# Kernel tuning notes

Hardware: AMD Instinct MI355X
Metric: run time of the kernel (lower is better)

The kernel has to match this reference:

```python
import jax, jax.numpy as jnp
import numpy as np

B, C, N = 16, 256, 8192          # batch, channels, points
CN, CL = 128, 64                 # curve_num, curve_length
MID = C // 2
BN_EPS = 1e-5


def setup_inputs() -> dict:
    key = jax.random.key(0)
    ks = jax.random.split(key, 10)
    def w(k, shape, fan_in):  # kaiming-ish init for 1x1 conv weights
        return jax.random.normal(k, shape, jnp.float32) * np.float32(1.0 / np.sqrt(fan_in))
    return {
        "x": jax.random.normal(ks[0], (B, C, N), jnp.float32),
        "curves": jax.random.normal(ks[1], (B, C, CN, CL), jnp.float32),
        "w_att": w(ks[2], (1, C), C),        # line_conv_att (Conv2d C->1, 1x1)
        "wa": w(ks[3], (MID, C), C),         # conva
        "wb": w(ks[4], (MID, C), C),         # convb
        "wc": w(ks[5], (MID, C), C),         # convc
        "wn": w(ks[6], (MID, MID), MID),     # convn
        "wl": w(ks[7], (MID, MID), MID),     # convl
        "wd": w(ks[8], (C, 2 * MID), 2 * MID),  # convd conv
        "bn_gamma": jnp.ones((C,), jnp.float32),
        "bn_beta": jnp.zeros((C,), jnp.float32),
        "bn_mean": jnp.zeros((C,), jnp.float32),
        "bn_var": jnp.ones((C,), jnp.float32),
    }


def reference(x, curves, w_att, wa, wb, wc, wn, wl, wd,
              bn_gamma, bn_beta, bn_mean, bn_var):
    # curves: [B, C, n, l]; attention logits over curves via 1x1 conv C->1
    att = jnp.einsum('oc,bcnl->bnl', w_att, curves)              # [B, n, l]
    # inter: softmax over curve_length (l); intra: softmax over curve_num (n)
    curver_inter = jnp.einsum('bcnl,bnl->bcn', curves, jax.nn.softmax(att, axis=-1))  # [B,C,n]
    curves_intra = jnp.einsum('bcnl,bnl->bcl', curves, jax.nn.softmax(att, axis=-2))  # [B,C,l]

    a = jnp.einsum('mc,bcn->bmn', wa, curver_inter)              # [B, mid, n]
    b = jnp.einsum('mc,bcl->bml', wb, curves_intra)              # [B, mid, l]
    x_logits = jnp.einsum('mc,bcp->bpm', wc, x)                  # [B, N, mid]

    x_inter = jax.nn.softmax(jnp.einsum('bpm,bmn->bpn', x_logits, a), axis=-1)  # [B,N,n]
    x_intra = jax.nn.softmax(jnp.einsum('bpm,bml->bpl', x_logits, b), axis=-1)  # [B,N,l]

    an = jnp.einsum('om,bmn->bno', wn, a)                        # [B, n, mid]
    bl = jnp.einsum('om,bml->blo', wl, b)                        # [B, l, mid]

    xi = jnp.einsum('bpn,bnm->bpm', x_inter, an)                 # [B, N, mid]
    xt = jnp.einsum('bpl,blm->bpm', x_intra, bl)                 # [B, N, mid]

    feat = jnp.concatenate((xi, xt), axis=-1)                    # [B, N, 2*mid]
    y = jnp.einsum('cd,bpd->bcp', wd, feat)                      # [B, C, N]
    # BatchNorm1d (inference mode: running stats)
    scale = (bn_gamma / jnp.sqrt(bn_var + BN_EPS))[None, :, None]
    y = (y - bn_mean[None, :, None]) * scale + bn_beta[None, :, None]
    return jax.nn.leaky_relu(x + y, 0.2)
```

## Files before the change

### kernel.cpp

```cpp
#include <hip/hip_runtime.h>
#include <hip/hip_bf16.h>
#include <cstdint>

#define B_   16
#define C_   256
#define N_   8192
#define CN_  128
#define CL_  64
#define MID_ 128

typedef unsigned short u16;
typedef __attribute__((ext_vector_type(8))) short bf8;
typedef __attribute__((ext_vector_type(4))) float f4;

#define MFMA(a, bb, c) __builtin_amdgcn_mfma_f32_16x16x32_bf16(a, bb, c, 0, 0, 0)

#define BAR() do {                                        \
    __builtin_amdgcn_sched_barrier(0);                    \
    asm volatile("s_waitcnt lgkmcnt(0)" ::: "memory");    \
    __builtin_amdgcn_s_barrier();                         \
    __builtin_amdgcn_sched_barrier(0);                    \
  } while (0)

__device__ inline u16 f2b(float v) {
  uint32_t b = __builtin_bit_cast(uint32_t, v);
  uint32_t r = (b + 0x7FFFu + ((b >> 16) & 1u)) >> 16;
  return (u16)r;
}
__device__ inline float b2f(u16 u) {
  uint32_t b = ((uint32_t)u) << 16;
  return __builtin_bit_cast(float, b);
}
__device__ inline void st4(u16* p, u16 a, u16 b, u16 c, u16 d) {
  unsigned long long v = (unsigned long long)a | ((unsigned long long)b << 16) |
                         ((unsigned long long)c << 32) | ((unsigned long long)d << 48);
  *(unsigned long long*)p = v;
}

__global__ __launch_bounds__(256) void k_wfold(const float* __restrict__ wd,
                                               const float* __restrict__ wn,
                                               const float* __restrict__ wl,
                                               float* __restrict__ wdnT,
                                               float* __restrict__ wdlT) {
  const int idx = blockIdx.x * 256 + threadIdx.x;
  const int plane = idx >> 15;
  const int r = idx & 32767;
  const int c = r & 255, m = r >> 8;
  const float* wsrc = plane ? wl : wn;
  const float* wdrow = wd + c * 256 + plane * 128;
  float a0 = 0.f, a1 = 0.f, a2 = 0.f, a3 = 0.f;
  for (int o = 0; o < 128; o += 4) {
    a0 = fmaf(wdrow[o + 0], wsrc[(o + 0) * 128 + m], a0);
    a1 = fmaf(wdrow[o + 1], wsrc[(o + 1) * 128 + m], a1);
    a2 = fmaf(wdrow[o + 2], wsrc[(o + 2) * 128 + m], a2);
    a3 = fmaf(wdrow[o + 3], wsrc[(o + 3) * 128 + m], a3);
  }
  (plane ? wdlT : wdnT)[m * 256 + c] = (a0 + a1) + (a2 + a3);
}

__global__ __launch_bounds__(256) void k_wfold2(
    const float* __restrict__ wa, const float* __restrict__ wb,
    const float* __restrict__ wc,
    const float* __restrict__ wdnT, const float* __restrict__ wdlT,
    float* __restrict__ Wac, float* __restrict__ Wna,
    float* __restrict__ Wbc, float* __restrict__ Wlb) {
  const int idx = blockIdx.x * 256 + threadIdx.x;
  const int quad = idx >> 16;
  const int r = idx & 65535;
  const int cc = r & 255, c = r >> 8;
  const float* L = (quad & 2) ? wb : wa;
  const float* R = (quad & 1) ? ((quad & 2) ? wdlT : wdnT) : wc;
  float a0 = 0.f, a1 = 0.f, a2 = 0.f, a3 = 0.f;
  for (int m = 0; m < 128; m += 4) {
    a0 = fmaf(L[(m + 0) * 256 + c], R[(m + 0) * 256 + cc], a0);
    a1 = fmaf(L[(m + 1) * 256 + c], R[(m + 1) * 256 + cc], a1);
    a2 = fmaf(L[(m + 2) * 256 + c], R[(m + 2) * 256 + cc], a2);
    a3 = fmaf(L[(m + 3) * 256 + c], R[(m + 3) * 256 + cc], a3);
  }
  float* O = (quad == 0) ? Wac : (quad == 1) ? Wna : (quad == 2) ? Wbc : Wlb;
  O[c * 256 + cc] = (a0 + a1) + (a2 + a3);
}

__global__ __launch_bounds__(256) void k_att(const float* __restrict__ curves,
                                             const float* __restrict__ w_att,
                                             float* __restrict__ attp) {
  const int blk = blockIdx.x;
  const int b = blk >> 6, seg = (blk >> 2) & 15, cs = blk & 3;
  const int e2 = seg * 512 + threadIdx.x * 2;
  const float* cb = curves + (size_t)b * C_ * CN_ * CL_ + (size_t)cs * 64 * 8192 + e2;
  const float* w = w_att + cs * 64;
  float2 a0 = {0.f, 0.f}, a1 = a0, a2 = a0, a3 = a0;
  #pragma unroll 4
  for (int c = 0; c < 64; c += 4) {
    const float w0 = w[c + 0], w1 = w[c + 1], w2 = w[c + 2], w3 = w[c + 3];
    float2 v0 = *(const float2*)&cb[(size_t)(c + 0) * 8192];
    float2 v1 = *(const float2*)&cb[(size_t)(c + 1) * 8192];
    float2 v2 = *(const float2*)&cb[(size_t)(c + 2) * 8192];
    float2 v3 = *(const float2*)&cb[(size_t)(c + 3) * 8192];
    a0.x = fmaf(w0, v0.x, a0.x); a0.y = fmaf(w0, v0.y, a0.y);
    a1.x = fmaf(w1, v1.x, a1.x); a1.y = fmaf(w1, v1.y, a1.y);
    a2.x = fmaf(w2, v2.x, a2.x); a2.y = fmaf(w2, v2.y, a2.y);
    a3.x = fmaf(w3, v3.x, a3.x); a3.y = fmaf(w3, v3.y, a3.y);
  }
  float2 a;
  a.x = (a0.x + a1.x) + (a2.x + a3.x);
  a.y = (a0.y + a1.y) + (a2.y + a3.y);
  *(float2*)&attp[(size_t)(cs * 16 + b) * 8192 + e2] = a;
}

__global__ __launch_bounds__(256) void k_softmax(const float* __restrict__ attp,
                                                 float* __restrict__ smi,
                                                 float* __restrict__ sma) {
  __shared__ float T[CN_ * CL_];
  __shared__ float rmax[CN_], rrcp[CN_], cmax[CL_], crcp[CL_];
  const int b = blockIdx.x;
  const int tid = threadIdx.x;
  for (int idx = tid; idx < CN_ * CL_; idx += 256) {
    T[idx] = attp[(size_t)b * 8192 + idx]
           + attp[(size_t)(16 + b) * 8192 + idx]
           + attp[(size_t)(32 + b) * 8192 + idx]
           + attp[(size_t)(48 + b) * 8192 + idx];
  }
  __syncthreads();
  if (tid < 128) {
    const int n = tid;
    float mx = -1e30f;
    for (int l = 0; l < CL_; ++l) mx = fmaxf(mx, T[n * 64 + l]);
    float s = 0.f;
    for (int l = 0; l < CL_; ++l) s += __expf(T[n * 64 + l] - mx);
    rmax[n] = mx; rrcp[n] = 1.f / s;
  } else if (tid < 192) {
    const int l = tid - 128;
    float mx = -1e30f;
    for (int n = 0; n < CN_; ++n) mx = fmaxf(mx, T[n * 64 + l]);
    float s = 0.f;
    for (int n = 0; n < CN_; ++n) s += __expf(T[n * 64 + l] - mx);
    cmax[l] = mx; crcp[l] = 1.f / s;
  }
  __syncthreads();
  for (int idx = tid; idx < CN_ * CL_; idx += 256) {
    const int n = idx >> 6, l = idx & 63;
    const float v = T[idx];
    smi[b * 8192 + idx] = __expf(v - rmax[n]) * rrcp[n];
    sma[b * 8192 + idx] = __expf(v - cmax[l]) * crcp[l];
  }
}

__global__ __launch_bounds__(256) void k_agg(const float* __restrict__ curves,
                                             const float* __restrict__ smi,
                                             const float* __restrict__ sma,
                                             float* __restrict__ cinter,
                                             float* __restrict__ cintra) {
  __shared__ float P[CN_ * CL_];
  const int blk = blockIdx.x;
  const int b = blk >> 8, c = blk & 255;
  const int tid = threadIdx.x;
  const float* src = curves + (size_t)(b * 256 + c) * 8192;
  for (int i4 = tid; i4 < 2048; i4 += 256)
    *(float4*)&P[i4 * 4] = *(const float4*)&src[i4 * 4];
  __syncthreads();
  if (tid < 128) {
    const int n = tid;
    const float* sp = smi + (size_t)(b * 128 + n) * 64;
    float a[4] = {0.f, 0.f, 0.f, 0.f};
    for (int l0 = 0; l0 < 64; l0 += 4) {
      float4 pv = *(const float4*)&P[n * 64 + l0];
      float4 sv = *(const float4*)&sp[l0];
      a[0] = fmaf(pv.x, sv.x, a[0]);
      a[1] = fmaf(pv.y, sv.y, a[1]);
      a[2] = fmaf(pv.z, sv.z, a[2]);
      a[3] = fmaf(pv.w, sv.w, a[3]);
    }
    cinter[(size_t)(b * 256 + c) * 128 + n] = (a[0] + a[1]) + (a[2] + a[3]);
  } else if (tid < 192) {
    const int l = tid - 128;
    float a[4] = {0.f, 0.f, 0.f, 0.f};
    for (int n0 = 0; n0 < 128; n0 += 4) {
      a[0] = fmaf(P[(n0 + 0) * 64 + l], sma[(size_t)(b * 128 + n0 + 0) * 64 + l], a[0]);
      a[1] = fmaf(P[(n0 + 1) * 64 + l], sma[(size_t)(b * 128 + n0 + 1) * 64 + l], a[1]);
      a[2] = fmaf(P[(n0 + 2) * 64 + l], sma[(size_t)(b * 128 + n0 + 2) * 64 + l], a[2]);
      a[3] = fmaf(P[(n0 + 3) * 64 + l], sma[(size_t)(b * 128 + n0 + 3) * 64 + l], a[3]);
    }
    cintra[(size_t)(b * 256 + c) * 64 + l] = (a[0] + a[1]) + (a[2] + a[3]);
  }
}

__global__ __launch_bounds__(256) void k_fold(
    const float* __restrict__ cinter, const float* __restrict__ cintra,
    const float* __restrict__ Wac, const float* __restrict__ Wna,
    const float* __restrict__ Wbc, const float* __restrict__ Wlb,
    u16* __restrict__ AnH, u16* __restrict__ AnL,
    u16* __restrict__ BlH, u16* __restrict__ BlL,
    u16* __restrict__ Wy) {
  __shared__ float S1[64 * 65], S2[64 * 65];
  const int blk = blockIdx.x;
  const int b = blk / 24, tile = blk - b * 24;
  const int tid = threadIdx.x;
  const int r = tid & 63, c4 = tid >> 6;
  float acc[16];
  #pragma unroll
  for (int i = 0; i < 16; ++i) acc[i] = 0.f;

  int n0 = 0, c0 = 0, type;
  if (tile < 8)       { type = 0; n0 = (tile >> 2) * 64; c0 = (tile & 3) * 64; }
  else if (tile < 12) { type = 1; c0 = (tile - 8) * 64; }
  else if (tile < 20) { type = 2; c0 = ((tile - 12) >> 1) * 64; n0 = ((tile - 12) & 1) * 64; }
  else                { type = 3; c0 = (tile - 20) * 64; }

  const float* cib = cinter + (size_t)b * 32768;
  const float* ctb = cintra + (size_t)b * 16384;

  for (int kh = 0; kh < 4; ++kh) {
    __syncthreads();
    if (type == 0) {
      for (int it = 0; it < 16; ++it) {
        const int flat = it * 256 + tid, cl = flat >> 6, j = flat & 63;
        const int c = kh * 64 + cl;
        S1[cl * 65 + j] = Wac[c * 256 + c0 + j];
        S2[cl * 65 + j] = cib[c * 128 + n0 + j];
      }
    } else if (type == 1) {
      for (int it = 0; it < 16; ++it) {
        const int flat = it * 256 + tid, cl = flat >> 6, j = flat & 63;
        const int c = kh * 64 + cl;
        S1[cl * 65 + j] = Wbc[c * 256 + c0 + j];
        S2[cl * 65 + j] = ctb[c * 64 + j];
      }
    } else if (type == 2) {
      for (int it = 0; it < 16; ++it) {
        const int flat = it * 256 + tid, cl = flat >> 6, j = flat & 63;
        const int c = kh * 64 + cl;
        S1[cl * 65 + j] = cib[c * 128 + n0 + j];
        S2[cl * 65 + j] = Wna[c * 256 + c0 + j];
      }
    } else {
      for (int it = 0; it < 16; ++it) {
        const int flat = it * 256 + tid, cl = flat >> 6, j = flat & 63;
        const int c = kh * 64 + cl;
        S1[cl * 65 + j] = ctb[c * 64 + j];
        S2[cl * 65 + j] = Wlb[c * 256 + c0 + j];
      }
    }
    __syncthreads();
    for (int k = 0; k < 64; ++k) {
      const float va = S1[k * 65 + r];
      #pragma unroll
      for (int cc = 0; cc < 16; ++cc)
        acc[cc] = fmaf(va, S2[k * 65 + c4 * 16 + cc], acc[cc]);
    }
  }

  if (type == 0) {
    #pragma unroll
    for (int cc = 0; cc < 16; ++cc) {
      const float v = acc[cc];
      const u16 h = f2b(v);
      const size_t o = (size_t)b * 32768 + (n0 + c4 * 16 + cc) * 256 + c0 + r;
      AnH[o] = h; AnL[o] = f2b(v - b2f(h));
    }
  } else if (type == 1) {
    #pragma unroll
    for (int cc = 0; cc < 16; ++cc) {
      const float v = acc[cc];
      const u16 h = f2b(v);
      const size_t o = (size_t)b * 16384 + (c4 * 16 + cc) * 256 + c0 + r;
      BlH[o] = h; BlL[o] = f2b(v - b2f(h));
    }
  } else if (type == 2) {
    #pragma unroll
    for (int cc = 0; cc < 16; ++cc)
      Wy[(size_t)b * 49152 + (c0 + c4 * 16 + cc) * 192 + n0 + r] = f2b(acc[cc]);
  } else {
    #pragma unroll
    for (int cc = 0; cc < 16; ++cc)
      Wy[(size_t)b * 49152 + (c0 + c4 * 16 + cc) * 192 + 128 + r] = f2b(acc[cc]);
  }
}

__global__ __launch_bounds__(256, 2) void k_big(
    const float* __restrict__ x,
    const u16* __restrict__ AnH, const u16* __restrict__ AnL,
    const u16* __restrict__ BlH, const u16* __restrict__ BlL,
    const u16* __restrict__ Wy,
    const float* __restrict__ bng, const float* __restrict__ bnb,
    const float* __restrict__ bnm, const float* __restrict__ bnv,
    float* __restrict__ out) {
  __shared__ __align__(16) u16 LDS[33792];
  float* scL = (float*)(LDS + 32768);
  float* biL = (float*)(LDS + 33280);

  const int tid  = threadIdx.x;
  const int lane = tid & 63;
  const int wid  = tid >> 6;
  const int l15  = lane & 15;
  const int lg   = lane >> 4;
  const int p    = wid * 16 + l15;
  const int blk  = blockIdx.x;
  const int wg   = ((blk & 7) << 7) | (blk >> 3);
  const int b    = wg >> 6;
  const int p0g  = (wg & 63) << 7;
  const f4 zero4 = {0.f, 0.f, 0.f, 0.f};

  const u16* AnHb = AnH + ((size_t)b << 15);
  const u16* AnLb = AnL + ((size_t)b << 15);
  const u16* BlHb = BlH + ((size_t)b << 14);
  const u16* BlLb = BlL + ((size_t)b << 14);
  const u16* Wyb  = Wy  + (size_t)b * 49152;

  {
    const float scv = bng[tid] * rsqrtf(bnv[tid] + 1e-5f);
    scL[tid] = scv;
    biL[tid] = bnb[tid] - bnm[tid] * scv;
  }

  const int xp  = tid & 127;
  const int xkc = tid >> 7;
  const float* xb = x + (size_t)b * C_ * N_ + p0g;
  const int xswp = (xp >> 1) & 3;
  const int xo0 = xp * 32 + (((2 * xkc + 0) ^ xswp) * 8);
  const int xo1 = xp * 32 + (((2 * xkc + 1) ^ xswp) * 8);
  const u16* aSrc[6];
  int aLds[6];
  #pragma unroll
  for (int j = 0; j < 6; ++j) {
    const int cid = j * 256 + tid;
    const int plane = (cid >= 768) ? 1 : 0;
    const int rr = cid - plane * 768;
    const int row = rr >> 2, kc = rr & 3;
    const u16* base;
    if (row < 128) base = (plane ? AnLb : AnHb) + row * 256;
    else           base = (plane ? BlLb : BlHb) + (row - 128) * 256;
    aSrc[j] = base + 8 * (kc ^ ((row >> 1) & 3));
    aLds[j] = plane * 6144 + row * 32 + kc * 8;
  }
  const u16* wSrc[4];
  int wLds[4];
  #pragma unroll
  for (int j = 0; j < 4; ++j) {
    const int cid = j * 256 + tid;
    const int row = cid >> 2, kc = cid & 3;
    wSrc[j] = Wyb + row * 192 + 8 * (kc ^ ((row >> 1) & 3));
    wLds[j] = 24576 + row * 32 + kc * 8;
  }

  f4 accS[8][2], accA[4][2];
  #pragma unroll
  for (int t = 0; t < 8; ++t) { accS[t][0] = zero4; accS[t][1] = zero4; }
  #pragma unroll
  for (int t = 0; t < 4; ++t) { accA[t][0] = zero4; accA[t][1] = zero4; }

  bf8 aReg[6];
  float xRaw[2][16];

  #pragma unroll
  for (int j = 0; j < 6; ++j) aReg[j] = *(const bf8*)(aSrc[j]);
  #pragma unroll
  for (int jj = 0; jj < 16; ++jj)
    xRaw[0][jj] = xb[(size_t)(xkc * 16 + jj) * N_ + xp];
  #pragma unroll
  for (int j = 0; j < 6; ++j) *(bf8*)(LDS + aLds[j]) = aReg[j];
  {
    bf8 h0, h1;
    #pragma unroll
    for (int jj = 0; jj < 8; ++jj) {
      h0[jj] = (short)f2b(xRaw[0][jj]);
      h1[jj] = (short)f2b(xRaw[0][8 + jj]);
    }
    *(bf8*)(LDS + 12288 + xo0) = h0;
    *(bf8*)(LDS + 12288 + xo1) = h1;
  }
  #pragma unroll
  for (int jj = 0; jj < 16; ++jj)
    xRaw[1][jj] = xb[(size_t)(32 + xkc * 16 + jj) * N_ + xp];
  BAR();

  const int rswp = (p >> 1) & 3;
  #pragma unroll
  for (int q = 0; q < 8; ++q) {
    if (q < 7) {
      #pragma unroll
      for (int j = 0; j < 6; ++j) aReg[j] = *(const bf8*)(aSrc[j] + (q + 1) * 32);
    }
    if (q < 6) {
      #pragma unroll
      for (int jj = 0; jj < 16; ++jj)
        xRaw[q & 1][jj] = xb[(size_t)((q + 2) * 32 + xkc * 16 + jj) * N_ + xp];
    }
    const bf8 xh0 = *(const bf8*)(LDS + 12288 + p * 32 + ((lg ^ rswp) * 8));
    const bf8 xh1 = *(const bf8*)(LDS + 12288 + (p + 64) * 32 + ((lg ^ rswp) * 8));
    #pragma unroll
    for (int t = 0; t < 8; ++t) {
      const int row = t * 16 + l15;
      const int sw = 8 * (lg ^ ((row >> 1) & 3));
      const bf8 ah = *(const bf8*)(LDS + row * 32 + sw);
      const bf8 al = *(const bf8*)(LDS + 6144 + row * 32 + sw);
      accS[t][0] = MFMA(ah, xh0, accS[t][0]);
      accS[t][0] = MFMA(al, xh0, accS[t][0]);
      accS[t][1] = MFMA(ah, xh1, accS[t][1]);
      accS[t][1] = MFMA(al, xh1, accS[t][1]);
    }
    #pragma unroll
    for (int t = 0; t < 4; ++t) {
      const int row = 128 + t * 16 + l15;
      const int sw = 8 * (lg ^ ((row >> 1) & 3));
      const bf8 ah = *(const bf8*)(LDS + row * 32 + sw);
      const bf8 al = *(const bf8*)(LDS + 6144 + row * 32 + sw);
      accA[t][0] = MFMA(ah, xh0, accA[t][0]);
      accA[t][0] = MFMA(al, xh0, accA[t][0]);
      accA[t][1] = MFMA(ah, xh1, accA[t][1]);
      accA[t][1] = MFMA(al, xh1, accA[t][1]);
    }
    bf8 nh0, nh1;
    if (q < 7) {
      #pragma unroll
      for (int jj = 0; jj < 8; ++jj) {
        nh0[jj] = (short)f2b(xRaw[(q + 1) & 1][jj]);
        nh1[jj] = (short)f2b(xRaw[(q + 1) & 1][8 + jj]);
      }
    }
    BAR();
    if (q < 7) {
      #pragma unroll
      for (int j = 0; j < 6; ++j) *(bf8*)(LDS + aLds[j]) = aReg[j];
      *(bf8*)(LDS + 12288 + xo0) = nh0;
      *(bf8*)(LDS + 12288 + xo1) = nh1;
      BAR();
    }
  }

  bf8 wReg[4];
  #pragma unroll
  for (int j = 0; j < 4; ++j) wReg[j] = *(const bf8*)(wSrc[j]);

  u16* E = LDS;
  #pragma unroll
  for (int s = 0; s < 2; ++s) {
    const int ps = p + s * 64;
    float mx = -3.0e38f;
    #pragma unroll
    for (int t = 0; t < 8; ++t)
      #pragma unroll
      for (int r = 0; r < 4; ++r) mx = fmaxf(mx, accS[t][s][r]);
    mx = fmaxf(mx, __shfl_xor(mx, 16));
    mx = fmaxf(mx, __shfl_xor(mx, 32));
    float sum = 0.f;
    #pragma unroll
    for (int t = 0; t < 8; ++t)
      #pragma unroll
      for (int r = 0; r < 4; ++r) {
        const float e = __expf(accS[t][s][r] - mx);
        accS[t][s][r] = e; sum += e;
      }
    sum += __shfl_xor(sum, 16);
    sum += __shfl_xor(sum, 32);
    const float rcp = 1.f / sum;
    #pragma unroll
    for (int t = 0; t < 8; ++t) {
      const int j0 = t * 16 + lg * 4;
      const int chunk = j0 >> 3;
      const int csw = (chunk & ~7) | ((chunk & 7) ^ (ps & 7));
      st4(E + ps * 192 + csw * 8 + (j0 & 7),
          f2b(accS[t][s][0] * rcp), f2b(accS[t][s][1] * rcp),
          f2b(accS[t][s][2] * rcp), f2b(accS[t][s][3] * rcp));
    }
    float mx2 = -3.0e38f;
    #pragma unroll
    for (int t = 0; t < 4; ++t)
      #pragma unroll
      for (int r = 0; r < 4; ++r) mx2 = fmaxf(mx2, accA[t][s][r]);
    mx2 = fmaxf(mx2, __shfl_xor(mx2, 16));
    mx2 = fmaxf(mx2, __shfl_xor(mx2, 32));
    float sum2 = 0.f;
    #pragma unroll
    for (int t = 0; t < 4; ++t)
      #pragma unroll
      for (int r = 0; r < 4; ++r) {
        const float e = __expf(accA[t][s][r] - mx2);
        accA[t][s][r] = e; sum2 += e;
      }
    sum2 += __shfl_xor(sum2, 16);
    sum2 += __shfl_xor(sum2, 32);
    const float rcp2 = 1.f / sum2;
    #pragma unroll
    for (int t = 0; t < 4; ++t) {
      const int j0 = 128 + t * 16 + lg * 4;
      const int chunk = j0 >> 3;
      const int csw = (chunk & ~7) | ((chunk & 7) ^ (ps & 7));
      st4(E + ps * 192 + csw * 8 + (j0 & 7),
          f2b(accA[t][s][0] * rcp2), f2b(accA[t][s][1] * rcp2),
          f2b(accA[t][s][2] * rcp2), f2b(accA[t][s][3] * rcp2));
    }
  }
  #pragma unroll
  for (int j = 0; j < 4; ++j) *(bf8*)(LDS + wLds[j]) = wReg[j];
  BAR();

  f4 acc8[16][2];
  #pragma unroll
  for (int t = 0; t < 16; ++t) { acc8[t][0] = zero4; acc8[t][1] = zero4; }

  #pragma unroll
  for (int q = 0; q < 6; ++q) {
    if (q < 5) {
      #pragma unroll
      for (int j = 0; j < 4; ++j) wReg[j] = *(const bf8*)(wSrc[j] + (q + 1) * 32);
    }
    const int jchunk = q * 4 + lg;
    const int cs0 = (jchunk & ~7) | ((jchunk & 7) ^ (p & 7));
    const bf8 ef0 = *(const bf8*)(E + p * 192 + cs0 * 8);
    const bf8 ef1 = *(const bf8*)(E + (p + 64) * 192 + cs0 * 8);
    #pragma unroll
    for (int t = 0; t < 16; ++t) {
      const int row = t * 16 + l15;
      const int sw = 8 * (lg ^ ((row >> 1) & 3));
      const bf8 wf = *(const bf8*)(LDS + 24576 + row * 32 + sw);
      acc8[t][0] = MFMA(wf, ef0, acc8[t][0]);
      acc8[t][1] = MFMA(wf, ef1, acc8[t][1]);
    }
    BAR();
    if (q < 5) {
      #pragma unroll
      for (int j = 0; j < 4; ++j) *(bf8*)(LDS + wLds[j]) = wReg[j];
      BAR();
    }
  }

  const size_t pcol = (size_t)p0g + p;
  #pragma unroll
  for (int t = 0; t < 16; ++t) {
    #pragma unroll
    for (int r = 0; r < 4; ++r) {
      const int c = t * 16 + lg * 4 + r;
      const float sc = scL[c], bi = biL[c];
      const size_t o0 = (((size_t)b * 256 + c) << 13) + pcol;
      const float z0 = x[o0] + acc8[t][0][r] * sc + bi;
      out[o0] = z0 > 0.f ? z0 : 0.2f * z0;
      const size_t o1 = o0 + 64;
      const float z1 = x[o1] + acc8[t][1][r] * sc + bi;
      out[o1] = z1 > 0.f ? z1 : 0.2f * z1;
    }
  }
}

extern "C" void kernel_launch(void* const* d_in, const int* in_sizes, int n_in,
                              void* d_out, int out_size, void* d_ws, size_t ws_size,
                              hipStream_t stream) {
  const float* x      = (const float*)d_in[0];
  const float* curves = (const float*)d_in[1];
  const float* w_att  = (const float*)d_in[2];
  const float* wa     = (const float*)d_in[3];
  const float* wb     = (const float*)d_in[4];
  const float* wc     = (const float*)d_in[5];
  const float* wn     = (const float*)d_in[6];
  const float* wl     = (const float*)d_in[7];
  const float* wd     = (const float*)d_in[8];
  const float* bng    = (const float*)d_in[9];
  const float* bnb    = (const float*)d_in[10];
  const float* bnm    = (const float*)d_in[11];
  const float* bnv    = (const float*)d_in[12];
  float* out = (float*)d_out;
  float* ws  = (float*)d_ws;

  float* smi    = ws + 131072;
  float* sma    = ws + 262144;
  float* cinter = ws + 393216;
  float* cintra = ws + 917504;
  float* attp   = ws + 1179648;
  float* Wac    = ws + 1179648;
  float* Wna    = ws + 1245184;
  float* Wbc    = ws + 1310720;
  float* Wlb    = ws + 1376256;
  float* wdnT   = ws + 1441792;
  float* wdlT   = ws + 1474560;

  u16* wsb = (u16*)d_ws;
  u16* AnH = wsb;
  u16* AnL = wsb + 524288;
  u16* BlH = wsb + 1048576;
  u16* BlL = wsb + 1310720;
  u16* Wyp = wsb + 1572864;

  k_att    <<<dim3(B_ * 64),  dim3(256), 0, stream>>>(curves, w_att, attp);
  k_softmax<<<dim3(B_),       dim3(256), 0, stream>>>(attp, smi, sma);
  k_wfold  <<<dim3(256),      dim3(256), 0, stream>>>(wd, wn, wl, wdnT, wdlT);
  k_wfold2 <<<dim3(1024),     dim3(256), 0, stream>>>(wa, wb, wc, wdnT, wdlT,
                                                      Wac, Wna, Wbc, Wlb);
  k_agg    <<<dim3(B_ * C_),  dim3(256), 0, stream>>>(curves, smi, sma, cinter, cintra);
  k_fold   <<<dim3(B_ * 24),  dim3(256), 0, stream>>>(cinter, cintra,
                                                      Wac, Wna, Wbc, Wlb,
                                                      AnH, AnL, BlH, BlL, Wyp);
  k_big    <<<dim3(1024),     dim3(256), 0, stream>>>(x, AnH, AnL, BlH, BlL, Wyp,
                                                      bng, bnb, bnm, bnv, out);
}
```

Before: 240.1 us.

## Stream A/B operand tiles directly to double-buffered LDS via global_load_lds

Replaces the register-staged global-to-LDS copy of the An/Bl operand tiles with direct global_load_lds DMA into a double-buffered LDS region. The x tile moves to a separate LDS offset. This frees the aReg registers and drops the LDS write step after the barrier. The aim is to overlap operand loads with MFMA work and lower register pressure. The cost is twice the LDS footprint for the A tiles, and the __syncthreads must correctly order the asynchronous LDS writes.

```diff
diff --git a/kernel.cpp b/kernel.cpp
--- a/kernel.cpp
+++ b/kernel.cpp
@@ -21,6 +21,12 @@
     __builtin_amdgcn_s_barrier();                         \
     __builtin_amdgcn_sched_barrier(0);                    \
   } while (0)
+
+__device__ inline void gll16(const void* g, void* l) {
+  __builtin_amdgcn_global_load_lds(
+      (const __attribute__((address_space(1))) void*)g,
+      (__attribute__((address_space(3))) void*)l, 16, 0, 0);
+}
 
 __device__ inline u16 f2b(float v) {
   uint32_t b = __builtin_bit_cast(uint32_t, v);
@@ -317,10 +323,10 @@
   const int xkc = tid >> 7;
   const float* xb = x + (size_t)b * C_ * N_ + p0g;
   const int xswp = (xp >> 1) & 3;
-  const int xo0 = xp * 32 + (((2 * xkc + 0) ^ xswp) * 8);
-  const int xo1 = xp * 32 + (((2 * xkc + 1) ^ xswp) * 8);
+  const int xo0 = 24576 + xp * 32 + (((2 * xkc + 0) ^ xswp) * 8);
+  const int xo1 = 24576 + xp * 32 + (((2 * xkc + 1) ^ xswp) * 8);
+
   const u16* aSrc[6];
-  int aLds[6];
   #pragma unroll
   for (int j = 0; j < 6; ++j) {
     const int cid = j * 256 + tid;
@@ -331,8 +337,11 @@
     if (row < 128) base = (plane ? AnLb : AnHb) + row * 256;
     else           base = (plane ? BlLb : BlHb) + (row - 128) * 256;
     aSrc[j] = base + 8 * (kc ^ ((row >> 1) & 3));
-    aLds[j] = plane * 6144 + row * 32 + kc * 8;
-  }
+  }
+  int aDstW[6];
+  #pragma unroll
+  for (int j = 0; j < 6; ++j) aDstW[j] = 8 * (j * 256 + wid * 64);
+
   const u16* wSrc[4];
   int wLds[4];
   #pragma unroll
@@ -349,16 +358,13 @@
   #pragma unroll
   for (int t = 0; t < 4; ++t) { accA[t][0] = zero4; accA[t][1] = zero4; }
 
-  bf8 aReg[6];
   float xRaw[2][16];
 
   #pragma unroll
-  for (int j = 0; j < 6; ++j) aReg[j] = *(const bf8*)(aSrc[j]);
+  for (int j = 0; j < 6; ++j) gll16(aSrc[j], LDS + aDstW[j]);
   #pragma unroll
   for (int jj = 0; jj < 16; ++jj)
     xRaw[0][jj] = xb[(size_t)(xkc * 16 + jj) * N_ + xp];
-  #pragma unroll
-  for (int j = 0; j < 6; ++j) *(bf8*)(LDS + aLds[j]) = aReg[j];
   {
     bf8 h0, h1;
     #pragma unroll
@@ -366,34 +372,37 @@
       h0[jj] = (short)f2b(xRaw[0][jj]);
       h1[jj] = (short)f2b(xRaw[0][8 + jj]);
     }
-    *(bf8*)(LDS + 12288 + xo0) = h0;
-    *(bf8*)(LDS + 12288 + xo1) = h1;
+    *(bf8*)(LDS + xo0) = h0;
+    *(bf8*)(LDS + xo1) = h1;
   }
   #pragma unroll
   for (int jj = 0; jj < 16; ++jj)
     xRaw[1][jj] = xb[(size_t)(32 + xkc * 16 + jj) * N_ + xp];
-  BAR();
+  __syncthreads();
 
   const int rswp = (p >> 1) & 3;
   #pragma unroll
   for (int q = 0; q < 8; ++q) {
+    const int cbuf = (q & 1) * 12288;
     if (q < 7) {
-      #pragma unroll
-      for (int j = 0; j < 6; ++j) aReg[j] = *(const bf8*)(aSrc[j] + (q + 1) * 32);
+      const int nbuf = ((q + 1) & 1) * 12288;
+      #pragma unroll
+      for (int j = 0; j < 6; ++j)
+        gll16(aSrc[j] + (q + 1) * 32, LDS + nbuf + aDstW[j]);
     }
     if (q < 6) {
       #pragma unroll
       for (int jj = 0; jj < 16; ++jj)
         xRaw[q & 1][jj] = xb[(size_t)((q + 2) * 32 + xkc * 16 + jj) * N_ + xp];
     }
-    const bf8 xh0 = *(const bf8*)(LDS + 12288 + p * 32 + ((lg ^ rswp) * 8));
-    const bf8 xh1 = *(const bf8*)(LDS + 12288 + (p + 64) * 32 + ((lg ^ rswp) * 8));
+    const bf8 xh0 = *(const bf8*)(LDS + 24576 + p * 32 + ((lg ^ rswp) * 8));
+    const bf8 xh1 = *(const bf8*)(LDS + 24576 + (p + 64) * 32 + ((lg ^ rswp) * 8));
     #pragma unroll
     for (int t = 0; t < 8; ++t) {
       const int row = t * 16 + l15;
       const int sw = 8 * (lg ^ ((row >> 1) & 3));
-      const bf8 ah = *(const bf8*)(LDS + row * 32 + sw);
-      const bf8 al = *(const bf8*)(LDS + 6144 + row * 32 + sw);
+      const bf8 ah = *(const bf8*)(LDS + cbuf + row * 32 + sw);
+      const bf8 al = *(const bf8*)(LDS + cbuf + 6144 + row * 32 + sw);
       accS[t][0] = MFMA(ah, xh0, accS[t][0]);
       accS[t][0] = MFMA(al, xh0, accS[t][0]);
       accS[t][1] = MFMA(ah, xh1, accS[t][1]);
@@ -403,8 +412,8 @@
     for (int t = 0; t < 4; ++t) {
       const int row = 128 + t * 16 + l15;
       const int sw = 8 * (lg ^ ((row >> 1) & 3));
-      const bf8 ah = *(const bf8*)(LDS + row * 32 + sw);
-      const bf8 al = *(const bf8*)(LDS + 6144 + row * 32 + sw);
+      const bf8 ah = *(const bf8*)(LDS + cbuf + row * 32 + sw);
+      const bf8 al = *(const bf8*)(LDS + cbuf + 6144 + row * 32 + sw);
       accA[t][0] = MFMA(ah, xh0, accA[t][0]);
       accA[t][0] = MFMA(al, xh0, accA[t][0]);
       accA[t][1] = MFMA(ah, xh1, accA[t][1]);
@@ -418,12 +427,10 @@
         nh1[jj] = (short)f2b(xRaw[(q + 1) & 1][8 + jj]);
       }
     }
-    BAR();
+    __syncthreads();
     if (q < 7) {
-      #pragma unroll
-      for (int j = 0; j < 6; ++j) *(bf8*)(LDS + aLds[j]) = aReg[j];
-      *(bf8*)(LDS + 12288 + xo0) = nh0;
-      *(bf8*)(LDS + 12288 + xo1) = nh1;
+      *(bf8*)(LDS + xo0) = nh0;
+      *(bf8*)(LDS + xo1) = nh1;
       BAR();
     }
   }
```

Result: no change. 237.6 us (-1.1%).
